# Performance work log

Measured on AMD Instinct MI355X. Metric: run time of the kernel, lower is better.

Reference implementation:

```python
import jax, jax.numpy as jnp
import numpy as np

NUM_CHARS = 28
MAX_LEN = 16
NUM_WORDS = 1000
BSZ = 2
SEQ = 32


def setup_inputs() -> dict:
    key = jax.random.key(0)
    k1, k2, k3, k4 = jax.random.split(key, 4)
    # dictionary words: char ids in [1, NUM_CHARS), padded with 0 past the word length
    word_lengths = jax.random.randint(k1, (NUM_WORDS,), 3, MAX_LEN + 1).astype(jnp.int32)
    word_lengths = word_lengths.at[0].set(MAX_LEN)  # torch asserts max(word_lengths) == x.shape[-1]
    pos = jnp.arange(MAX_LEN)
    wchars = jax.random.randint(k2, (NUM_WORDS, MAX_LEN), 1, NUM_CHARS).astype(jnp.int32)
    words = jnp.where(pos[None, :] < word_lengths[:, None], wchars, 0)
    # input words: lengths < MAX_LEN so argmin over chars (pad=0) recovers the length, as the torch code relies on
    xlen = jax.random.randint(k3, (BSZ, SEQ), 3, MAX_LEN)
    xchars = jax.random.randint(k4, (BSZ, SEQ, MAX_LEN), 1, NUM_CHARS).astype(jnp.int32)
    x = jnp.where(pos[None, None, :] < xlen[:, :, None], xchars, 0)
    out_scale = jnp.ones((1,), jnp.float32)  # float passthrough (value 1.0, math-neutral)
    return {"x": x, "words": words, "word_lengths": word_lengths, "out_scale": out_scale}


def _forward(x, words, word_lengths, out_scale):
    bsz, seq, max_len = x.shape
    num_words = words.shape[0]
    s = out_scale[0]
    # torch: m, sequence_word_lengths = x.min(dim=-1)  -> argmin (pad char 0 marks word end)
    seq_wl = jnp.argmin(x, axis=-1)  # (b, s) int
    wlf = word_lengths.astype(jnp.float32)
    max_dist = (seq_wl.astype(jnp.float32)[:, :, None] + wlf[None, None, :]) * s  # (b, s, nw)
    ar = jnp.arange(max_len, dtype=jnp.float32)
    # word_lengths_arranged[w, i] = i if i < word_lengths[w] else 0
    wla = jnp.where(ar[None, :] < wlf[:, None], ar[None, :], 0.0) * s          # (nw, ml)
    swl = jnp.where(ar[None, None, :] < seq_wl[:, :, None], ar[None, None, :], 0.0) * s  # (b, s, ml)

    d = jnp.zeros((bsz, seq, num_words, max_len + 2, max_len + 2), jnp.float32)
    d = d.at[:, :, :, 1, 2:].set(wla[None, None])
    d = d.at[:, :, :, 2:, 1].set(swl[:, :, None, :])
    d = d.at[:, :, :, 0, :].set(max_dist[..., None])
    d = d.at[:, :, :, :, 0].set(max_dist[..., None])

    da = jnp.zeros((NUM_CHARS + 2,), jnp.float32)  # F.pad(zeros(num_chars), (2, 0))
    for i in range(1, max_len + 1):
        db = jnp.zeros((bsz, seq, num_words), jnp.float32)
        xi = x[:, :, i - 2]  # static negative index wraps, matching torch
        for j in range(1, max_len + 1):
            wj = words[:, j - 2]            # (nw,)
            k = da[wj]                      # (nw,) float, last-seen row per word char
            l = db                          # (b, s, nw) float, from previous j
            # d_transpose[b,s,w] = d[b, s, w, int(k[w]), int(l[b,s,w])]
            li = jnp.broadcast_to(l.astype(jnp.int32)[..., None, None],
                                  (bsz, seq, num_words, max_len + 2, 1))
            t = jnp.take_along_axis(d, li, axis=4)[..., 0]          # (b, s, nw, ml+2)
            ki = jnp.broadcast_to(k.astype(jnp.int32)[None, None, :, None],
                                  (bsz, seq, num_words, 1))
            d_trans = jnp.take_along_axis(t, ki, axis=3)[..., 0]    # (b, s, nw)
            # torch _total_combination_eq: 1 where chars differ, 0 where equal
            cost = (xi[:, :, None] != wj[None, None, :]).astype(jnp.float32)
            db = (1.0 - cost) * j
            trans = d_trans + (i - k[None, None, :] - 1.0) + 1.0 + (j - l - 1.0)
            cell = jnp.minimum(
                jnp.minimum(d[:, :, :, i - 1, j] + 1.0, d[:, :, :, i, j - 1] + 1.0),
                jnp.minimum(d[:, :, :, i - 1, j - 1] + cost, trans))
            d = d.at[:, :, :, i, j].set(cell)
            da = da.at[xi].set(jnp.float32(i))  # shared scatter across the whole batch, as in torch
    # final gather: d[b, s, w, word_lengths[w] + 1, seq_wl[b, s] + 1]
    row = jnp.broadcast_to((word_lengths.astype(jnp.int32) + 1)[None, None, :, None, None],
                           (bsz, seq, num_words, 1, max_len + 2))
    lev = jnp.take_along_axis(d, row, axis=3)[:, :, :, 0, :]        # (b, s, nw, ml+2)
    col = jnp.broadcast_to((seq_wl.astype(jnp.int32) + 1)[:, :, None, None],
                           (bsz, seq, num_words, 1))
    lev = jnp.take_along_axis(lev, col, axis=3)[..., 0]             # (b, s, nw)
    return lev


def reference(x, words, word_lengths, out_scale):
    return _forward(x, words, word_lengths, out_scale)
```

## Files before the change

kernel.cpp:

```cpp
#include <hip/hip_runtime.h>

#define ML 16
#define NW 1000
#define NBS 64

__global__ __launch_bounds__(64) void build_cm_kernel(const int* __restrict__ x,
                                                      unsigned* __restrict__ cm_g) {
    __shared__ unsigned cm[32];
    const int t = threadIdx.x;
    if (t < 32) cm[t] = 0u;
    __syncthreads();
    const int* xr = x + t * ML;
    #pragma unroll
    for (int p = 0; p < ML; ++p) {
        int c = xr[p];
        int i = (p <= 14) ? (p + 2) : 1;
        atomicOr(&cm[c], 1u << i);
    }
    __syncthreads();
    if (t < 32) cm_g[t] = cm[t];
}

__global__ __launch_bounds__(64) void dl_dp_kernel(
    const int* __restrict__ x,
    const int* __restrict__ words,
    const int* __restrict__ word_lengths,
    const float* __restrict__ out_scale,
    const unsigned* __restrict__ cm_g,
    float* __restrict__ out)
{
    const int lane = threadIdx.x;
    const int bs = blockIdx.x >> 4;
    const int chunk = blockIdx.x & 15;
    const int w_raw = chunk * 64 + lane;
    const bool active = (w_raw < NW);
    const int w = active ? w_raw : (NW - 1);
    const float s = out_scale[0];

    const int* xr = x + bs * ML;
    int xc[ML];
    #pragma unroll
    for (int p = 0; p < ML; ++p) xc[p] = xr[p];
    int minv = xc[0], seq_wl = 0;
    #pragma unroll
    for (int p = 1; p < ML; ++p)
        if (xc[p] < minv) { minv = xc[p]; seq_wl = p; }

    int wc[ML];
    const int4* wp = (const int4*)(words + w * ML);
    int4 q0 = wp[0], q1 = wp[1], q2 = wp[2], q3 = wp[3];
    wc[0]=q0.x; wc[1]=q0.y; wc[2]=q0.z; wc[3]=q0.w;
    wc[4]=q1.x; wc[5]=q1.y; wc[6]=q1.z; wc[7]=q1.w;
    wc[8]=q2.x; wc[9]=q2.y; wc[10]=q2.z; wc[11]=q2.w;
    wc[12]=q3.x; wc[13]=q3.y; wc[14]=q3.z; wc[15]=q3.w;

    unsigned rm[ML];
    #pragma unroll
    for (int t = 0; t < ML; ++t) rm[t] = cm_g[wc[t]];

    const int wl = word_lengths[w];
    const float maxdist = (float)(seq_wl + wl) * s;

    float prev[ML], tb[15], mk[ML];
    #pragma unroll
    for (int j = 0; j < ML; ++j) prev[j] = maxdist;
    #pragma unroll
    for (int t = 0; t < 15; ++t) tb[t] = maxdist;
    #pragma unroll
    for (int t = 0; t < ML; ++t) mk[t] = maxdist;

    float res = 0.0f;
    const int sq1 = seq_wl + 1;
    const int rowcap = wl + 1;

    int xi_next = xr[15];
    #pragma unroll 1
    for (int i = 1; i <= ML; ++i) {
        const int xi = xi_next;
        if (i < ML) xi_next = xr[(i - 1) & 15];
        const float fi = (float)i;
        const float md_i = maxdist - fi;

        bool b[ML];
        #pragma unroll
        for (int t = 0; t < ML; ++t) b[t] = ((rm[t] >> i) & 1u) != 0u;
        #pragma unroll
        for (int t = 0; t < 15; ++t) if (b[t]) mk[t] = md_i;
        const bool hit_row = (i == rowcap);

        const bool eq1 = (xi == wc[15]);
        const float cost1 = eq1 ? 0.0f : 1.0f;
        const float trans1 = mk[15] + fi;
        float cell = fminf(fminf(prev[0] + 1.0f, maxdist + 1.0f),
                           fminf(maxdist + cost1, trans1));
        if (b[15]) mk[15] = md_i;
        bool pm = eq1;
        float left = cell;
        float cur[ML];
        cur[0] = cell;
        if (b[0]) tb[0] = cell - fi;
        if (hit_row && sq1 == 1) res = cell;

        #pragma unroll
        for (int j = 2; j <= ML; ++j) {
            const int t = j - 2;
            const bool eq = (xi == wc[t]);
            const float cost = eq ? 0.0f : 1.0f;
            const float trans_l0 = mk[t] + (float)(i + j - 1);
            const float trans_ln = b[t] ? left : (tb[t] + fi);
            const float trans = pm ? trans_ln : trans_l0;
            const float up = prev[j - 1];
            const float diag = prev[j - 2];
            const float cellv = fminf(fminf(up + 1.0f, left + 1.0f),
                                      fminf(diag + cost, trans));
            cur[j - 1] = cellv;
            if (j <= 15 && b[j - 1]) tb[j - 1] = cellv - fi;
            if (hit_row && j == sq1) res = cellv;
            pm = eq;
            left = cellv;
        }
        #pragma unroll
        for (int j = 0; j < ML; ++j) prev[j] = cur[j];
    }

    if (active) out[bs * NW + w] = res;
}

extern "C" void kernel_launch(void* const* d_in, const int* in_sizes, int n_in,
                              void* d_out, int out_size, void* d_ws, size_t ws_size,
                              hipStream_t stream) {
    const int*   x            = (const int*)d_in[0];
    const int*   words        = (const int*)d_in[1];
    const int*   word_lengths = (const int*)d_in[2];
    const float* out_scale    = (const float*)d_in[3];
    float*       out          = (float*)d_out;
    unsigned*    cm           = (unsigned*)d_ws;

    build_cm_kernel<<<dim3(1), dim3(64), 0, stream>>>(x, cm);
    dl_dp_kernel<<<dim3(NBS * 16), dim3(64), 0, stream>>>(
        x, words, word_lengths, out_scale, cm, out);
}
```

Before: 74.02 us.

## Fuse char-mask build into DP kernel and widen blocks to 256 threads

Removes the separate single-block kernel that built the per-character position bitmask. Each 256-thread block now rebuilds the mask in shared memory and reads it from there instead of global memory. Blocks are widened from 64 to 256 threads with four waves per block, and the input row is read from registers inside the loop. This removes one launch and the dependency between the two kernels, at the cost of every block redoing the small mask build behind a barrier. There is also a dynamic register-array index (xc[(i-1)&15]) that may spill to scratch.

```diff
diff --git a/kernel.cpp b/kernel.cpp
--- a/kernel.cpp
+++ b/kernel.cpp
@@ -4,38 +4,36 @@
 #define NW 1000
 #define NBS 64
 
-__global__ __launch_bounds__(64) void build_cm_kernel(const int* __restrict__ x,
-                                                      unsigned* __restrict__ cm_g) {
-    __shared__ unsigned cm[32];
-    const int t = threadIdx.x;
-    if (t < 32) cm[t] = 0u;
-    __syncthreads();
-    const int* xr = x + t * ML;
-    #pragma unroll
-    for (int p = 0; p < ML; ++p) {
-        int c = xr[p];
-        int i = (p <= 14) ? (p + 2) : 1;
-        atomicOr(&cm[c], 1u << i);
-    }
-    __syncthreads();
-    if (t < 32) cm_g[t] = cm[t];
-}
-
-__global__ __launch_bounds__(64) void dl_dp_kernel(
+__global__ __launch_bounds__(256) void dl_fused_kernel(
     const int* __restrict__ x,
     const int* __restrict__ words,
     const int* __restrict__ word_lengths,
     const float* __restrict__ out_scale,
-    const unsigned* __restrict__ cm_g,
     float* __restrict__ out)
 {
-    const int lane = threadIdx.x;
-    const int bs = blockIdx.x >> 4;
-    const int chunk = blockIdx.x & 15;
+    __shared__ unsigned cm[32];
+    const int tid = threadIdx.x;
+    const int lane = tid & 63;
+    const int wv = tid >> 6;
+    const int bs = blockIdx.x >> 2;
+    const int chunk = (blockIdx.x & 3) * 4 + wv;
     const int w_raw = chunk * 64 + lane;
     const bool active = (w_raw < NW);
     const int w = active ? w_raw : (NW - 1);
     const float s = out_scale[0];
+
+    if (tid < 32) cm[tid] = 0u;
+    __syncthreads();
+    if (tid < 64) {
+        const int* xq = x + tid * ML;
+        #pragma unroll
+        for (int p = 0; p < ML; ++p) {
+            int c = xq[p];
+            int i = (p <= 14) ? (p + 2) : 1;
+            atomicOr(&cm[c], 1u << i);
+        }
+    }
+    __syncthreads();
 
     const int* xr = x + bs * ML;
     int xc[ML];
@@ -56,7 +54,7 @@
 
     unsigned rm[ML];
     #pragma unroll
-    for (int t = 0; t < ML; ++t) rm[t] = cm_g[wc[t]];
+    for (int t = 0; t < ML; ++t) rm[t] = cm[wc[t]];
 
     const int wl = word_lengths[w];
     const float maxdist = (float)(seq_wl + wl) * s;
@@ -73,11 +71,11 @@
     const int sq1 = seq_wl + 1;
     const int rowcap = wl + 1;
 
-    int xi_next = xr[15];
+    int xi_next = xc[15];
     #pragma unroll 1
     for (int i = 1; i <= ML; ++i) {
         const int xi = xi_next;
-        if (i < ML) xi_next = xr[(i - 1) & 15];
+        if (i < ML) xi_next = xc[(i - 1) & 15];
         const float fi = (float)i;
         const float md_i = maxdist - fi;
 
@@ -134,9 +132,7 @@
     const int*   word_lengths = (const int*)d_in[2];
     const float* out_scale    = (const float*)d_in[3];
     float*       out          = (float*)d_out;
-    unsigned*    cm           = (unsigned*)d_ws;
 
-    build_cm_kernel<<<dim3(1), dim3(64), 0, stream>>>(x, cm);
-    dl_dp_kernel<<<dim3(NBS * 16), dim3(64), 0, stream>>>(
-        x, words, word_lengths, out_scale, cm, out);
+    dl_fused_kernel<<<dim3(NBS * 4), dim3(256), 0, stream>>>(
+        x, words, word_lengths, out_scale, out);
 }
```

Result: faster. 71.24 us (-3.7%).
